# Kernel tuning notes

Hardware: AMD Instinct MI355X
Metric: run time of the kernel (lower is better)

Reference implementation:

```python
import jax, jax.numpy as jnp
import numpy as np

COMMITMENT = 1.0

def setup_inputs() -> dict:
    key = jax.random.key(0)
    k1, k2 = jax.random.split(key)
    x = jax.random.normal(k1, (32, 64, 64, 64), dtype=jnp.float32)       # [B, D, H, W]
    emb_w = jax.random.normal(k2, (512, 64), dtype=jnp.float32)          # [K, D] codebook
    return {"x": x, "emb_w": emb_w}

def reference(x, emb_w):
    B, D, H, W = x.shape
    K = emb_w.shape[0]
    # permute channels last and flatten: [B*H*W, D]
    xp = jnp.transpose(x, (0, 2, 3, 1))
    flat = xp.reshape(-1, D)
    # squared-distance matrix [N, K] via ||a||^2 + ||b||^2 - 2 a.b
    distances = (jnp.sum(flat * flat, axis=1, keepdims=True)
                 + jnp.sum(emb_w * emb_w, axis=1)
                 - 2.0 * jnp.matmul(flat, emb_w.T))
    encoding_flat = jnp.argmin(distances, axis=1)                        # [N]
    quantized = emb_w[encoding_flat].reshape(B, H, W, D)                 # gather
    quantized = jnp.transpose(quantized, (0, 3, 1, 2))                   # back to [B, D, H, W]
    # commitment loss: mse(stop_grad(quantized), x)
    e_latent_loss = jnp.mean((jax.lax.stop_gradient(quantized) - x) ** 2)
    loss = COMMITMENT * e_latent_loss
    # straight-through estimator
    quantized_st = x + jax.lax.stop_gradient(quantized - x)
    encoding = encoding_flat.reshape(B, H, W)
    return quantized_st, encoding, distances, loss
```

## Files before the change

### kernel.cpp

```cpp
#include <hip/hip_runtime.h>

typedef short short8 __attribute__((ext_vector_type(8)));
typedef float f32x4 __attribute__((ext_vector_type(4)));

#define EPS 0.012f

__device__ __forceinline__ unsigned short rne_bf16(float v) {
    unsigned u = __float_as_uint(v);
    unsigned r = u + 0x7FFFu + ((u >> 16) & 1u);
    return (unsigned short)(r >> 16);
}
__device__ __forceinline__ float bf16_to_f(unsigned short h) {
    return __uint_as_float(((unsigned)h) << 16);
}

#define MFMA(a,b,c) __builtin_amdgcn_mfma_f32_16x16x32_bf16((a),(b),(c),0,0,0)

#define LIGHT_BARRIER() do {                                   \
    asm volatile("s_waitcnt lgkmcnt(0)" ::: "memory");         \
    __builtin_amdgcn_s_barrier();                              \
    __builtin_amdgcn_sched_barrier(0);                         \
} while (0)

__global__ __launch_bounds__(64) void prep_kernel(
    const float* __restrict__ emb, unsigned short* __restrict__ whi,
    unsigned short* __restrict__ wlo, float* __restrict__ wee)
{
    const int k = blockIdx.x * 64 + threadIdx.x;
    const float* src = emb + k * 64;
    float nrm = 0.f;
    #pragma unroll
    for (int g = 0; g < 8; ++g) {
        float4 v0 = *(const float4*)(src + g * 8);
        float4 v1 = *(const float4*)(src + g * 8 + 4);
        float vv[8] = {v0.x, v0.y, v0.z, v0.w, v1.x, v1.y, v1.z, v1.w};
        short8 h8, l8;
        #pragma unroll
        for (int i = 0; i < 8; ++i) {
            nrm = fmaf(vv[i], vv[i], nrm);
            float v2 = -2.0f * vv[i];
            unsigned short hb = rne_bf16(v2);
            h8[i] = (short)hb;
            l8[i] = (short)rne_bf16(v2 - bf16_to_f(hb));
        }
        *(short8*)(whi + k * 64 + g * 8) = h8;
        *(short8*)(wlo + k * 64 + g * 8) = l8;
    }
    wee[k] = nrm;
}

#define DT 36

__global__ __launch_bounds__(256, 4) void vq_kernel(
    const float* __restrict__ x, const float* __restrict__ emb,
    const unsigned short* __restrict__ whi, const unsigned short* __restrict__ wlo,
    const float* __restrict__ wee,
    float* __restrict__ out_q, float* __restrict__ out_enc,
    float* __restrict__ out_dist, float* __restrict__ out_loss)
{
    __shared__ __align__(16) unsigned short ehi[2][32 * 64];
    __shared__ __align__(16) unsigned short elo[2][32 * 64];
    __shared__ __align__(16) float dtile[4][16 * DT];
    __shared__ __align__(16) float ee_s[512];
    __shared__ int   enc_s[64];
    __shared__ float red_s[4];

    const int t   = threadIdx.x;
    const int bid = blockIdx.x;
    const int n_base = bid * 64;
    const size_t xbase = (size_t)(bid >> 6) * 262144 + (size_t)(bid & 63) * 64;
    const int l  = t & 63;
    const int wv = t >> 6;

    ee_s[t]       = wee[t];
    ee_s[t + 256] = wee[t + 256];

    const int myw = wv * 16 + (l & 15);
    const int g8  = (l >> 4) * 8;
    float va[16];
    {
        const float* xp = x + xbase + myw;
        #pragma unroll
        for (int i = 0; i < 8; ++i) {
            va[i]     = xp[(size_t)(g8 + i) * 4096];
            va[8 + i] = xp[(size_t)(g8 + 32 + i) * 4096];
        }
    }
    short8 xhi0, xhi1, xlo0, xlo1;
    float xx = 0.f;
    #pragma unroll
    for (int i = 0; i < 8; ++i) {
        xx = fmaf(va[i], va[i], xx);
        xx = fmaf(va[8 + i], va[8 + i], xx);
        unsigned short hb = rne_bf16(va[i]);
        xhi0[i] = (short)hb; xlo0[i] = (short)rne_bf16(va[i] - bf16_to_f(hb));
        unsigned short hb2 = rne_bf16(va[8 + i]);
        xhi1[i] = (short)hb2; xlo1[i] = (short)rne_bf16(va[8 + i] - bf16_to_f(hb2));
    }
    xx += __shfl_xor(xx, 16, 64);
    xx += __shfl_xor(xx, 32, 64);
    const f32x4 xx4 = {xx, xx, xx, xx};

    short8 sh, sl;
    const int skr = t >> 3;
    const int sd0 = (t & 7) * 8;
    const int sidx = skr * 64 + (sd0 ^ ((skr & 7) << 3));
    #define STAGE_LOAD(c) {                                                    \
        sh = *(const short8*)(whi + (size_t)(((c) * 32 + skr) * 64 + sd0));    \
        sl = *(const short8*)(wlo + (size_t)(((c) * 32 + skr) * 64 + sd0));    \
    }
    #define STAGE_WRITE(bufi) {                                                \
        *(short8*)&ehi[bufi][sidx] = sh;                                       \
        *(short8*)&elo[bufi][sidx] = sl;                                       \
    }

    STAGE_LOAD(0); STAGE_WRITE(0);
    float m1 = 3.4e38f, m2 = 3.4e38f; int k1 = 0;
    const int colb = (l >> 4) * 4;
    float* dwv = dtile[wv];
    __syncthreads();

    #pragma unroll 2
    for (int c = 0; c < 16; ++c) {
        if (c < 15) STAGE_LOAD(c + 1);
        const int bufi = c & 1;
        #pragma unroll
        for (int kti = 0; kti < 2; ++kti) {
            const int krl = kti * 16 + (l & 15);
            const int sw  = (krl & 7) << 3;
            const int bix = krl * 64;
            short8 ch0 = *(short8*)&ehi[bufi][bix + (g8 ^ sw)];
            short8 ch1 = *(short8*)&ehi[bufi][bix + ((g8 + 32) ^ sw)];
            short8 cl0 = *(short8*)&elo[bufi][bix + (g8 ^ sw)];
            short8 cl1 = *(short8*)&elo[bufi][bix + ((g8 + 32) ^ sw)];
            const int kb = c * 32 + kti * 16 + colb;
            f32x4 accA = *(const f32x4*)&ee_s[kb];
            f32x4 accB = xx4;
            accA = MFMA(ch0, xhi0, accA);
            accB = MFMA(ch1, xhi1, accB);
            accA = MFMA(cl0, xhi0, accA);
            accB = MFMA(cl1, xhi1, accB);
            accA = MFMA(ch0, xlo0, accA);
            accB = MFMA(ch1, xlo1, accB);
            f32x4 dist4;
            #pragma unroll
            for (int r = 0; r < 4; ++r) {
                float dv = accA[r] + accB[r];
                dist4[r] = dv;
                float nm2 = fmaxf(fminf(dv, m2), m1);
                int  kidx = kb | r;
                k1 = (dv < m1) ? kidx : k1;
                m1 = fminf(dv, m1);
                m2 = nm2;
            }
            *(f32x4*)&dwv[(l & 15) * DT + (kti * 4 + (l >> 4)) * 4] = dist4;
        }
        #pragma unroll
        for (int p = 0; p < 2; ++p) {
            const int row = p * 8 + (l >> 3);
            const int k4  = (l & 7) * 4;
            f32x4 v = *(f32x4*)&dwv[row * DT + k4];
            *(f32x4*)(out_dist + (size_t)(n_base + wv * 16 + row) * 512 + c * 32 + k4) = v;
        }
        if (c < 15) STAGE_WRITE((c + 1) & 1);
        LIGHT_BARRIER();
    }

    __syncthreads();

    float* drow = out_dist + (size_t)(n_base + myw) * 512;
    float bv = m1; int bk = k1;
    {
        float ov = __shfl_xor(bv, 16, 64); int ok = __shfl_xor(bk, 16, 64);
        if (ov < bv || (ov == bv && ok < bk)) { bv = ov; bk = ok; }
        ov = __shfl_xor(bv, 32, 64); ok = __shfl_xor(bk, 32, 64);
        if (ov < bv || (ov == bv && ok < bk)) { bv = ov; bk = ok; }
    }
    const float thr = bv + EPS;
    const unsigned long long gmask = 0x0001000100010001ULL << (l & 15);
    unsigned long long b1 = __ballot(m1 <= thr);
    unsigned long long b2 = __ballot(m2 <= thr);
    int enc = bk; float lossv = bv;
    if (__popcll(b1 & gmask) > 1 || (b2 & gmask) != 0ULL) {
        const float* dr   = drow + (l >> 4) * 128;
        const float* xcol = x + xbase + myw;
        double bestv = 1e300; int bestk = 0x7fffffff;
        #pragma unroll 1
        for (int c4 = 0; c4 < 32; ++c4) {
            float4 dv4 = *(const float4*)(dr + c4 * 4);
            float dvv[4] = {dv4.x, dv4.y, dv4.z, dv4.w};
            #pragma unroll 1
            for (int j = 0; j < 4; ++j) {
                if (dvv[j] <= thr) {
                    int k = (l >> 4) * 128 + c4 * 4 + j;
                    const float* er = emb + k * 64;
                    double s = 0.0;
                    #pragma unroll 4
                    for (int d = 0; d < 64; ++d) {
                        double df = (double)xcol[(size_t)d * 4096] - (double)er[d];
                        s += df * df;
                    }
                    if (s < bestv) { bestv = s; bestk = k; }
                }
            }
        }
        double ov = __shfl_xor(bestv, 16, 64); int ok = __shfl_xor(bestk, 16, 64);
        if (ov < bestv || (ov == bestv && ok < bestk)) { bestv = ov; bestk = ok; }
        ov = __shfl_xor(bestv, 32, 64); ok = __shfl_xor(bestk, 32, 64);
        if (ov < bestv || (ov == bestv && ok < bestk)) { bestv = ov; bestk = ok; }
        enc = bestk;
        if (l < 16 && enc != bk) lossv = drow[enc];
    }
    if (l < 16) {
        enc_s[myw] = enc;
        out_enc[n_base + myw] = (float)enc;
    }
    float lc = (l < 16) ? lossv : 0.f;
    #pragma unroll
    for (int m = 32; m >= 1; m >>= 1) lc += __shfl_down(lc, m, 64);
    if (l == 0) red_s[wv] = lc;
    __syncthreads();
    if (t == 0)
        atomicAdd(out_loss, (red_s[0] + red_s[1] + red_s[2] + red_s[3]) * (1.0f / 8388608.0f));

    {
        const int w  = t & 63;
        const int dg = t >> 6;
        const int e  = enc_s[w];
        const float* er = emb + e * 64 + dg * 16;
        float* qp = out_q + xbase + (size_t)(dg * 16) * 4096 + w;
        #pragma unroll
        for (int qi = 0; qi < 4; ++qi) {
            float4 q4 = *(const float4*)(er + qi * 4);
            qp[(size_t)(qi * 4 + 0) * 4096] = q4.x;
            qp[(size_t)(qi * 4 + 1) * 4096] = q4.y;
            qp[(size_t)(qi * 4 + 2) * 4096] = q4.z;
            qp[(size_t)(qi * 4 + 3) * 4096] = q4.w;
        }
    }
}

extern "C" void kernel_launch(void* const* d_in, const int* in_sizes, int n_in,
                              void* d_out, int out_size, void* d_ws, size_t ws_size,
                              hipStream_t stream) {
    const float* x   = (const float*)d_in[0];
    const float* emb = (const float*)d_in[1];

    float* out_q    = (float*)d_out;
    float* out_enc  = out_q + 8388608;
    float* out_dist = out_enc + 131072;
    float* out_loss = out_dist + 67108864;

    unsigned short* whi = (unsigned short*)d_ws;
    unsigned short* wlo = whi + 32768;
    float*          wee = (float*)(whi + 65536);

    hipMemsetAsync(out_loss, 0, sizeof(float), stream);
    prep_kernel<<<8, 64, 0, stream>>>(emb, whi, wlo, wee);
    vq_kernel<<<2048, 256, 0, stream>>>(x, emb, whi, wlo, wee,
                                        out_q, out_enc, out_dist, out_loss);
}
```

Baseline: 103.3 us.

## Process two image rows per block to reuse codebook tiles across more points

Each block now handles 128 points (two H rows) instead of 64. Every wave keeps bf16 hi/lo fragments for two sets of 16 points, so each codebook tile staged into LDS feeds twice the MFMA work. The grid halves to 1024 blocks. This amortizes the codebook staging and the per-block barrier overhead, but raises register pressure, which could reduce occupancy. The loop also drops to unroll 1, and the dist tile in LDS doubles in size.

```diff
diff --git a/kernel.cpp b/kernel.cpp
--- a/kernel.cpp
+++ b/kernel.cpp
@@ -60,15 +60,17 @@
 {
     __shared__ __align__(16) unsigned short ehi[2][32 * 64];
     __shared__ __align__(16) unsigned short elo[2][32 * 64];
-    __shared__ __align__(16) float dtile[4][16 * DT];
+    __shared__ __align__(16) float dtile[4][32 * DT];
     __shared__ __align__(16) float ee_s[512];
-    __shared__ int   enc_s[64];
+    __shared__ int   enc_s[128];
     __shared__ float red_s[4];
 
     const int t   = threadIdx.x;
     const int bid = blockIdx.x;
-    const int n_base = bid * 64;
-    const size_t xbase = (size_t)(bid >> 6) * 262144 + (size_t)(bid & 63) * 64;
+    const int n_base = bid * 128;
+    const int b   = bid >> 5;
+    const int h0  = (bid & 31) * 2;
+    const size_t xb0 = (size_t)b * 262144 + (size_t)h0 * 64;
     const int l  = t & 63;
     const int wv = t >> 6;
 
@@ -77,29 +79,47 @@
 
     const int myw = wv * 16 + (l & 15);
     const int g8  = (l >> 4) * 8;
-    float va[16];
+    short8 xhiA0, xhiA1, xloA0, xloA1, xhiB0, xhiB1, xloB0, xloB1;
+    float xxA = 0.f, xxB = 0.f;
     {
-        const float* xp = x + xbase + myw;
-        #pragma unroll
-        for (int i = 0; i < 8; ++i) {
-            va[i]     = xp[(size_t)(g8 + i) * 4096];
-            va[8 + i] = xp[(size_t)(g8 + 32 + i) * 4096];
-        }
-    }
-    short8 xhi0, xhi1, xlo0, xlo1;
-    float xx = 0.f;
-    #pragma unroll
-    for (int i = 0; i < 8; ++i) {
-        xx = fmaf(va[i], va[i], xx);
-        xx = fmaf(va[8 + i], va[8 + i], xx);
-        unsigned short hb = rne_bf16(va[i]);
-        xhi0[i] = (short)hb; xlo0[i] = (short)rne_bf16(va[i] - bf16_to_f(hb));
-        unsigned short hb2 = rne_bf16(va[8 + i]);
-        xhi1[i] = (short)hb2; xlo1[i] = (short)rne_bf16(va[8 + i] - bf16_to_f(hb2));
-    }
-    xx += __shfl_xor(xx, 16, 64);
-    xx += __shfl_xor(xx, 32, 64);
-    const f32x4 xx4 = {xx, xx, xx, xx};
+        float va[16];
+        const float* xpA = x + xb0 + myw;
+        #pragma unroll
+        for (int i = 0; i < 8; ++i) {
+            va[i]     = xpA[(size_t)(g8 + i) * 4096];
+            va[8 + i] = xpA[(size_t)(g8 + 32 + i) * 4096];
+        }
+        #pragma unroll
+        for (int i = 0; i < 8; ++i) {
+            xxA = fmaf(va[i], va[i], xxA);
+            xxA = fmaf(va[8 + i], va[8 + i], xxA);
+            unsigned short hb = rne_bf16(va[i]);
+            xhiA0[i] = (short)hb; xloA0[i] = (short)rne_bf16(va[i] - bf16_to_f(hb));
+            unsigned short hb2 = rne_bf16(va[8 + i]);
+            xhiA1[i] = (short)hb2; xloA1[i] = (short)rne_bf16(va[8 + i] - bf16_to_f(hb2));
+        }
+        const float* xpB = x + xb0 + 64 + myw;
+        #pragma unroll
+        for (int i = 0; i < 8; ++i) {
+            va[i]     = xpB[(size_t)(g8 + i) * 4096];
+            va[8 + i] = xpB[(size_t)(g8 + 32 + i) * 4096];
+        }
+        #pragma unroll
+        for (int i = 0; i < 8; ++i) {
+            xxB = fmaf(va[i], va[i], xxB);
+            xxB = fmaf(va[8 + i], va[8 + i], xxB);
+            unsigned short hb = rne_bf16(va[i]);
+            xhiB0[i] = (short)hb; xloB0[i] = (short)rne_bf16(va[i] - bf16_to_f(hb));
+            unsigned short hb2 = rne_bf16(va[8 + i]);
+            xhiB1[i] = (short)hb2; xloB1[i] = (short)rne_bf16(va[8 + i] - bf16_to_f(hb2));
+        }
+    }
+    xxA += __shfl_xor(xxA, 16, 64);
+    xxA += __shfl_xor(xxA, 32, 64);
+    xxB += __shfl_xor(xxB, 16, 64);
+    xxB += __shfl_xor(xxB, 32, 64);
+    const f32x4 xx4A = {xxA, xxA, xxA, xxA};
+    const f32x4 xx4B = {xxB, xxB, xxB, xxB};
 
     short8 sh, sl;
     const int skr = t >> 3;
@@ -115,12 +135,13 @@
     }
 
     STAGE_LOAD(0); STAGE_WRITE(0);
-    float m1 = 3.4e38f, m2 = 3.4e38f; int k1 = 0;
+    float m1[2] = {3.4e38f, 3.4e38f}, m2[2] = {3.4e38f, 3.4e38f};
+    int   k1[2] = {0, 0};
     const int colb = (l >> 4) * 4;
     float* dwv = dtile[wv];
     __syncthreads();
 
-    #pragma unroll 2
+    #pragma unroll 1
     for (int c = 0; c < 16; ++c) {
         if (c < 15) STAGE_LOAD(c + 1);
         const int bufi = c & 1;
@@ -134,33 +155,56 @@
             short8 cl0 = *(short8*)&elo[bufi][bix + (g8 ^ sw)];
             short8 cl1 = *(short8*)&elo[bufi][bix + ((g8 + 32) ^ sw)];
             const int kb = c * 32 + kti * 16 + colb;
-            f32x4 accA = *(const f32x4*)&ee_s[kb];
-            f32x4 accB = xx4;
-            accA = MFMA(ch0, xhi0, accA);
-            accB = MFMA(ch1, xhi1, accB);
-            accA = MFMA(cl0, xhi0, accA);
-            accB = MFMA(cl1, xhi1, accB);
-            accA = MFMA(ch0, xlo0, accA);
-            accB = MFMA(ch1, xlo1, accB);
-            f32x4 dist4;
-            #pragma unroll
-            for (int r = 0; r < 4; ++r) {
-                float dv = accA[r] + accB[r];
-                dist4[r] = dv;
-                float nm2 = fmaxf(fminf(dv, m2), m1);
-                int  kidx = kb | r;
-                k1 = (dv < m1) ? kidx : k1;
-                m1 = fminf(dv, m1);
-                m2 = nm2;
+            f32x4 ee4 = *(const f32x4*)&ee_s[kb];
+            const int qoff = (kti * 4 + (l >> 4)) * 4;
+            {
+                f32x4 aA = ee4, aB = xx4A;
+                aA = MFMA(ch0, xhiA0, aA);
+                aB = MFMA(ch1, xhiA1, aB);
+                aA = MFMA(cl0, xhiA0, aA);
+                aB = MFMA(cl1, xhiA1, aB);
+                aA = MFMA(ch0, xloA0, aA);
+                aB = MFMA(ch1, xloA1, aB);
+                f32x4 d4;
+                #pragma unroll
+                for (int r = 0; r < 4; ++r) {
+                    float dv = aA[r] + aB[r];
+                    d4[r] = dv;
+                    float nm2 = fmaxf(fminf(dv, m2[0]), m1[0]);
+                    k1[0] = (dv < m1[0]) ? (kb | r) : k1[0];
+                    m1[0] = fminf(dv, m1[0]);
+                    m2[0] = nm2;
+                }
+                *(f32x4*)&dwv[(l & 15) * DT + qoff] = d4;
             }
-            *(f32x4*)&dwv[(l & 15) * DT + (kti * 4 + (l >> 4)) * 4] = dist4;
-        }
-        #pragma unroll
-        for (int p = 0; p < 2; ++p) {
+            {
+                f32x4 aA = ee4, aB = xx4B;
+                aA = MFMA(ch0, xhiB0, aA);
+                aB = MFMA(ch1, xhiB1, aB);
+                aA = MFMA(cl0, xhiB0, aA);
+                aB = MFMA(cl1, xhiB1, aB);
+                aA = MFMA(ch0, xloB0, aA);
+                aB = MFMA(ch1, xloB1, aB);
+                f32x4 d4;
+                #pragma unroll
+                for (int r = 0; r < 4; ++r) {
+                    float dv = aA[r] + aB[r];
+                    d4[r] = dv;
+                    float nm2 = fmaxf(fminf(dv, m2[1]), m1[1]);
+                    k1[1] = (dv < m1[1]) ? (kb | r) : k1[1];
+                    m1[1] = fminf(dv, m1[1]);
+                    m2[1] = nm2;
+                }
+                *(f32x4*)&dwv[(16 + (l & 15)) * DT + qoff] = d4;
+            }
+        }
+        #pragma unroll
+        for (int p = 0; p < 4; ++p) {
             const int row = p * 8 + (l >> 3);
             const int k4  = (l & 7) * 4;
             f32x4 v = *(f32x4*)&dwv[row * DT + k4];
-            *(f32x4*)(out_dist + (size_t)(n_base + wv * 16 + row) * 512 + c * 32 + k4) = v;
+            const int grow = (row >> 4) * 64 + wv * 16 + (row & 15);
+            *(f32x4*)(out_dist + (size_t)(n_base + grow) * 512 + c * 32 + k4) = v;
         }
         if (c < 15) STAGE_WRITE((c + 1) & 1);
         LIGHT_BARRIER();
@@ -168,54 +212,59 @@
 
     __syncthreads();
 
-    float* drow = out_dist + (size_t)(n_base + myw) * 512;
-    float bv = m1; int bk = k1;
-    {
-        float ov = __shfl_xor(bv, 16, 64); int ok = __shfl_xor(bk, 16, 64);
-        if (ov < bv || (ov == bv && ok < bk)) { bv = ov; bk = ok; }
-        ov = __shfl_xor(bv, 32, 64); ok = __shfl_xor(bk, 32, 64);
-        if (ov < bv || (ov == bv && ok < bk)) { bv = ov; bk = ok; }
-    }
-    const float thr = bv + EPS;
     const unsigned long long gmask = 0x0001000100010001ULL << (l & 15);
-    unsigned long long b1 = __ballot(m1 <= thr);
-    unsigned long long b2 = __ballot(m2 <= thr);
-    int enc = bk; float lossv = bv;
-    if (__popcll(b1 & gmask) > 1 || (b2 & gmask) != 0ULL) {
-        const float* dr   = drow + (l >> 4) * 128;
-        const float* xcol = x + xbase + myw;
-        double bestv = 1e300; int bestk = 0x7fffffff;
-        #pragma unroll 1
-        for (int c4 = 0; c4 < 32; ++c4) {
-            float4 dv4 = *(const float4*)(dr + c4 * 4);
-            float dvv[4] = {dv4.x, dv4.y, dv4.z, dv4.w};
+    float lc = 0.f;
+    #pragma unroll 1
+    for (int s = 0; s < 2; ++s) {
+        const int grow = s * 64 + wv * 16 + (l & 15);
+        float* drow = out_dist + (size_t)(n_base + grow) * 512;
+        float bv = m1[s]; int bk = k1[s];
+        {
+            float ov = __shfl_xor(bv, 16, 64); int ok = __shfl_xor(bk, 16, 64);
+            if (ov < bv || (ov == bv && ok < bk)) { bv = ov; bk = ok; }
+            ov = __shfl_xor(bv, 32, 64); ok = __shfl_xor(bk, 32, 64);
+            if (ov < bv || (ov == bv && ok < bk)) { bv = ov; bk = ok; }
+        }
+        const float thr = bv + EPS;
+        unsigned long long b1 = __ballot(m1[s] <= thr);
+        unsigned long long b2 = __ballot(m2[s] <= thr);
+        int enc = bk; float lossv = bv;
+        if (__popcll(b1 & gmask) > 1 || (b2 & gmask) != 0ULL) {
+            const float* dr   = drow + (l >> 4) * 128;
+            const float* xcol = x + xb0 + s * 64 + myw;
+            double bestv = 1e300; int bestk = 0x7fffffff;
             #pragma unroll 1
-            for (int j = 0; j < 4; ++j) {
-                if (dvv[j] <= thr) {
-                    int k = (l >> 4) * 128 + c4 * 4 + j;
-                    const float* er = emb + k * 64;
-                    double s = 0.0;
-                    #pragma unroll 4
-                    for (int d = 0; d < 64; ++d) {
-                        double df = (double)xcol[(size_t)d * 4096] - (double)er[d];
-                        s += df * df;
+            for (int c4 = 0; c4 < 32; ++c4) {
+                float4 dv4 = *(const float4*)(dr + c4 * 4);
+                float dvv[4] = {dv4.x, dv4.y, dv4.z, dv4.w};
+                #pragma unroll 1
+                for (int j = 0; j < 4; ++j) {
+                    if (dvv[j] <= thr) {
+                        int k = (l >> 4) * 128 + c4 * 4 + j;
+                        const float* er = emb + k * 64;
+                        double sum = 0.0;
+                        #pragma unroll 4
+                        for (int d = 0; d < 64; ++d) {
+                            double df = (double)xcol[(size_t)d * 4096] - (double)er[d];
+                            sum += df * df;
+                        }
+                        if (sum < bestv) { bestv = sum; bestk = k; }
                     }
-                    if (s < bestv) { bestv = s; bestk = k; }
                 }
             }
-        }
-        double ov = __shfl_xor(bestv, 16, 64); int ok = __shfl_xor(bestk, 16, 64);
-        if (ov < bestv || (ov == bestv && ok < bestk)) { bestv = ov; bestk = ok; }
-        ov = __shfl_xor(bestv, 32, 64); ok = __shfl_xor(bestk, 32, 64);
-        if (ov < bestv || (ov == bestv && ok < bestk)) { bestv = ov; bestk = ok; }
-        enc = bestk;
-        if (l < 16 && enc != bk) lossv = drow[enc];
-    }
-    if (l < 16) {
-        enc_s[myw] = enc;
-        out_enc[n_base + myw] = (float)enc;
-    }
-    float lc = (l < 16) ? lossv : 0.f;
+            double ov = __shfl_xor(bestv, 16, 64); int ok = __shfl_xor(bestk, 16, 64);
+            if (ov < bestv || (ov == bestv && ok < bestk)) { bestv = ov; bestk = ok; }
+            ov = __shfl_xor(bestv, 32, 64); ok = __shfl_xor(bestk, 32, 64);
+            if (ov < bestv || (ov == bestv && ok < bestk)) { bestv = ov; bestk = ok; }
+            enc = bestk;
+            if (l < 16 && enc != bk) lossv = drow[enc];
+        }
+        if (l < 16) {
+            enc_s[grow] = enc;
+            out_enc[n_base + grow] = (float)enc;
+            lc += lossv;
+        }
+    }
     #pragma unroll
     for (int m = 32; m >= 1; m >>= 1) lc += __shfl_down(lc, m, 64);
     if (l == 0) red_s[wv] = lc;
@@ -226,16 +275,19 @@
     {
         const int w  = t & 63;
         const int dg = t >> 6;
-        const int e  = enc_s[w];
-        const float* er = emb + e * 64 + dg * 16;
-        float* qp = out_q + xbase + (size_t)(dg * 16) * 4096 + w;
-        #pragma unroll
-        for (int qi = 0; qi < 4; ++qi) {
-            float4 q4 = *(const float4*)(er + qi * 4);
-            qp[(size_t)(qi * 4 + 0) * 4096] = q4.x;
-            qp[(size_t)(qi * 4 + 1) * 4096] = q4.y;
-            qp[(size_t)(qi * 4 + 2) * 4096] = q4.z;
-            qp[(size_t)(qi * 4 + 3) * 4096] = q4.w;
+        #pragma unroll
+        for (int hh = 0; hh < 2; ++hh) {
+            const int e  = enc_s[hh * 64 + w];
+            const float* er = emb + e * 64 + dg * 16;
+            float* qp = out_q + xb0 + (size_t)(dg * 16) * 4096 + hh * 64 + w;
+            #pragma unroll
+            for (int qi = 0; qi < 4; ++qi) {
+                float4 q4 = *(const float4*)(er + qi * 4);
+                qp[(size_t)(qi * 4 + 0) * 4096] = q4.x;
+                qp[(size_t)(qi * 4 + 1) * 4096] = q4.y;
+                qp[(size_t)(qi * 4 + 2) * 4096] = q4.z;
+                qp[(size_t)(qi * 4 + 3) * 4096] = q4.w;
+            }
         }
     }
 }
@@ -257,6 +309,6 @@
 
     hipMemsetAsync(out_loss, 0, sizeof(float), stream);
     prep_kernel<<<8, 64, 0, stream>>>(emb, whi, wlo, wee);
-    vq_kernel<<<2048, 256, 0, stream>>>(x, emb, whi, wlo, wee,
+    vq_kernel<<<1024, 256, 0, stream>>>(x, emb, whi, wlo, wee,
                                         out_q, out_enc, out_dist, out_loss);
 }
```

After: 116.5 us. 12.7% more time.
